# Performance work log

Hardware: AMD Instinct MI355X
Metric: run time of the kernel (lower is better)

The kernel has to match this reference:

```python
import jax, jax.numpy as jnp
import numpy as np

DIM = 256          # channel dim
WIN = 16           # window_size
PW = WIN // 2      # permuted_window_size
N = PW * PW        # tokens per window = 64
H = 8              # num_heads
KV_DIM = DIM // 2  # compressed q/k/v dim = 128
HD = KV_DIM // H   # per-head compressed dim = 16
SCALE = (DIM // H) ** (-0.5)  # NOTE: scale uses UNcompressed head dim, as in source
B = 4096           # total windows (batch * num_windows)
NW = 64            # nw_mask; B % NW == 0


def _relative_position_index():
    coords = np.stack(np.meshgrid(np.arange(PW), np.arange(PW), indexing='ij'))  # [2,PW,PW]
    cf = coords.reshape(2, -1)                          # [2, N]
    rel = cf[:, :, None] - cf[:, None, :]               # [2, N, N]
    rel = rel.transpose(1, 2, 0).copy()                 # [N, N, 2]
    rel[:, :, 0] += PW - 1
    rel[:, :, 1] += PW - 1
    rel[:, :, 0] *= 2 * PW - 1
    return jnp.asarray(rel.sum(-1), dtype=jnp.int32)    # [N, N]


def setup_inputs() -> dict:
    key = jax.random.key(0)
    ks = jax.random.split(key, 9)
    std = 0.02
    return {
        'x': jax.random.normal(ks[0], (B, N, DIM), dtype=jnp.float32),
        'mask': jax.random.normal(ks[1], (NW, N, N), dtype=jnp.float32),
        'q_w': jax.random.normal(ks[2], (KV_DIM, DIM), dtype=jnp.float32) * std,
        'q_b': jnp.zeros((KV_DIM,), dtype=jnp.float32),
        'kv_w': jax.random.normal(ks[3], (2 * KV_DIM, DIM), dtype=jnp.float32) * std,
        'kv_b': jnp.zeros((2 * KV_DIM,), dtype=jnp.float32),
        'proj_w': jax.random.normal(ks[4], (DIM, KV_DIM), dtype=jnp.float32) * std,
        'proj_b': jnp.zeros((DIM,), dtype=jnp.float32),
        'bias_table': jax.random.normal(ks[5], ((2 * PW - 1) ** 2, H), dtype=jnp.float32) * std,
        'rel_index': _relative_position_index(),
    }


def reference(x, mask, q_w, q_b, kv_w, kv_b, proj_w, proj_b, bias_table, rel_index):
    b, n, c = x.shape
    # compressed Q and KV projections
    q = (x @ q_w.T + q_b).reshape(b, n, H, HD).transpose(0, 2, 1, 3)        # [B,H,N,HD]
    kv = (x @ kv_w.T + kv_b).reshape(b, n, 2, H, HD).transpose(2, 0, 3, 1, 4)
    k, v = kv[0], kv[1]                                                     # [B,H,N,HD]
    attn = jnp.einsum('bhnd,bhmd->bhnm', q, k) * SCALE                      # [B,H,N,N]
    # relative position bias gather
    bias = bias_table[rel_index.reshape(-1)].reshape(n, n, H).transpose(2, 0, 1)  # [H,N,N]
    attn = attn + bias[None]
    # window mask add: broadcast mask over (B//NW) window-batches and heads
    attn = attn.reshape(b // NW, NW, H, n, n) + mask[None, :, None]
    attn = attn.reshape(b, H, n, n)
    attn = jax.nn.softmax(attn, axis=-1)
    out = jnp.einsum('bhnm,bhmd->bhnd', attn, v)                            # [B,H,N,HD]
    out = out.transpose(0, 2, 1, 3).reshape(b, n, KV_DIM)
    return out @ proj_w.T + proj_b                                          # [B,N,DIM]
```

## Files before the change

kernel.cpp:

```cpp
#include <hip/hip_runtime.h>
#include <hip/hip_bf16.h>


typedef unsigned short u16;
typedef short bf16x8 __attribute__((ext_vector_type(8)));
typedef short bf16x4 __attribute__((ext_vector_type(4)));
typedef float f32x4  __attribute__((ext_vector_type(4)));

__device__ __forceinline__ f32x4 mfma_bf16(bf16x8 a, bf16x8 b, f32x4 c) {
  return __builtin_amdgcn_mfma_f32_16x16x32_bf16(a, b, c, 0, 0, 0);
}
__device__ __forceinline__ f32x4 mfma16(bf16x4 a, bf16x4 b, f32x4 c) {
#if __has_builtin(__builtin_amdgcn_mfma_f32_16x16x16bf16_1k)
  return __builtin_amdgcn_mfma_f32_16x16x16bf16_1k(a, b, c, 0, 0, 0);
#else
  f32x4 d;
  asm("v_mfma_f32_16x16x16_bf16 %0, %1, %2, %3" : "=v"(d) : "v"(a), "v"(b), "v"(c));
  return d;
#endif
}

#define SCALE_F 0.1767766952966369f
#define LOG2E_F 1.4426950408889634f
#define C2F (SCALE_F * LOG2E_F)

__device__ __forceinline__ u16 f2b(float f) {
  return __builtin_bit_cast(u16, __float2bfloat16(f));
}
__device__ __forceinline__ float b2f(u16 h) {
  return __builtin_bit_cast(float, (unsigned)h << 16);
}
__device__ __forceinline__ float fexp2(float x) {
#if __has_builtin(__builtin_amdgcn_exp2f)
  return __builtin_amdgcn_exp2f(x);
#else
  return __expf(x * 0.6931471805599453f);
#endif
}

#define WS_WQKV   0
#define WS_WPROJ  98304
#define WS_BIASPK 131072
#define WS_MASKPK 163840
#define WS_QKVB   425984
#define WS_TOTAL  426368

__global__ void psa_prep(const float* __restrict__ qw, const float* __restrict__ qb,
                         const float* __restrict__ kvw, const float* __restrict__ kvb,
                         const float* __restrict__ projw, const float* __restrict__ bt,
                         const int* __restrict__ ri, const float* __restrict__ mask,
                         u16* __restrict__ ws) {
  int i = blockIdx.x * 256 + threadIdx.x;
  if (i < 98304) {
    int r = i >> 8, c = i & 255;
    ws[WS_WQKV + i] = f2b(r < 128 ? qw[r * 256 + c] : kvw[(r - 128) * 256 + c]);
  } else if (i < 131072) {
    int j = i - 98304;
    ws[WS_WPROJ + j] = f2b(projw[j]);
  } else if (i < 163840) {
    int j = i - 131072;
    int t = j & 15, lane = (j >> 4) & 63, w = (j >> 10) & 3, h = j >> 12;
    int row = w * 16 + (lane & 15);
    int col = (t >> 2) * 16 + ((lane >> 4) & 3) * 4 + (t & 3);
    ws[WS_BIASPK + j] = f2b(LOG2E_F * bt[ri[row * 64 + col] * 8 + h]);
  } else if (i < 425984) {
    int j = i - 163840;
    int t = j & 15, lane = (j >> 4) & 63, w = (j >> 10) & 3, nw = j >> 12;
    int row = w * 16 + (lane & 15);
    int col = (t >> 2) * 16 + ((lane >> 4) & 3) * 4 + (t & 3);
    ws[WS_MASKPK + j] = f2b(LOG2E_F * mask[(nw * 64 + row) * 64 + col]);
  } else if (i < WS_TOTAL) {
    int j = i - 425984;
    ws[WS_QKVB + j] = f2b(j < 128 ? qb[j] : kvb[j - 128]);
  }
}

__global__ __launch_bounds__(256, 3) void psa_main(
    const float* __restrict__ x, const float* __restrict__ proj_b,
    const u16* __restrict__ ws, float* __restrict__ out) {
  __shared__ __align__(16) u16 qks[64 * 264];
  __shared__ __align__(16) u16 vsm[8 * 16 * 72];

  const int win = blockIdx.x;
  const int tid = threadIdx.x;
  const int wave = tid >> 6;
  const int lane = tid & 63;
  const int quad = lane >> 4;
  const int n16  = lane & 15;
  const int nw   = win & 63;

  const f32x4 zero4 = {0.f, 0.f, 0.f, 0.f};
  const float* xw = x + (size_t)win * 16384;

  #pragma unroll
  for (int it = 0; it < 16; ++it) {
    int idx = it * 256 + tid;
    int row = idx >> 6, c4 = (idx & 63) * 4;
    float4 v = *(const float4*)(xw + row * 256 + c4);
    bf16x4 pk;
    pk[0] = (short)f2b(v.x); pk[1] = (short)f2b(v.y);
    pk[2] = (short)f2b(v.z); pk[3] = (short)f2b(v.w);
    *(bf16x4*)&qks[row * 264 + c4] = pk;
  }
  __syncthreads();

  f32x4 acc[6][4];
  #pragma unroll
  for (int i = 0; i < 6; ++i)
    #pragma unroll
    for (int nt = 0; nt < 4; ++nt) acc[i][nt] = zero4;

  #pragma unroll 2
  for (int kk = 0; kk < 8; ++kk) {
    bf16x8 xf[4];
    #pragma unroll
    for (int nt = 0; nt < 4; ++nt)
      xf[nt] = *(const bf16x8*)&qks[(nt * 16 + n16) * 264 + kk * 32 + quad * 8];
    #pragma unroll
    for (int i = 0; i < 6; ++i) {
      int mt = wave + i * 4;
      bf16x8 wf = *(const bf16x8*)&ws[WS_WQKV + (mt * 16 + n16) * 256 + kk * 32 + quad * 8];
      #pragma unroll
      for (int nt = 0; nt < 4; ++nt) acc[i][nt] = mfma_bf16(wf, xf[nt], acc[i][nt]);
    }
  }
  __syncthreads();

  #pragma unroll
  for (int i = 0; i < 6; ++i) {
    int mt = wave + i * 4;
    bf16x4 bq = *(const bf16x4*)&ws[WS_QKVB + mt * 16 + quad * 4];
    float ba[4];
    #pragma unroll
    for (int r = 0; r < 4; ++r) ba[r] = b2f((u16)bq[r]);
    if (i < 4) {
      #pragma unroll
      for (int nt = 0; nt < 4; ++nt) {
        bf16x4 pk;
        #pragma unroll
        for (int r = 0; r < 4; ++r) pk[r] = (short)f2b(acc[i][nt][r] + ba[r]);
        *(bf16x4*)&qks[(nt * 16 + n16) * 264 + mt * 16 + quad * 4] = pk;
      }
    } else {
      #pragma unroll
      for (int nt = 0; nt < 4; ++nt)
        #pragma unroll
        for (int r = 0; r < 4; ++r)
          vsm[(mt - 16) * 1152 + (quad * 4 + r) * 72 + nt * 16 + n16] =
              f2b(acc[i][nt][r] + ba[r]);
    }
  }
  __syncthreads();

  const u16* bpk = ws + WS_BIASPK + (wave * 64 + lane) * 16;
  const u16* mpk = ws + WS_MASKPK + ((nw * 4 + wave) * 64 + lane) * 16;
  bf16x8 mm0 = *(const bf16x8*)mpk;
  bf16x8 mm1 = *(const bf16x8*)(mpk + 8);

  #pragma unroll 2
  for (int h = 0; h < 8; ++h) {
    bf16x4 qf = *(const bf16x4*)&qks[(wave * 16 + n16) * 264 + h * 16 + quad * 4];
    f32x4 s[4];
    #pragma unroll
    for (int nt = 0; nt < 4; ++nt) {
      bf16x4 kf = *(const bf16x4*)&qks[(nt * 16 + n16) * 264 + 128 + h * 16 + quad * 4];
      s[nt] = mfma16(kf, qf, zero4);
    }
    bf16x8 bm0 = *(const bf16x8*)(bpk + h * 4096);
    bf16x8 bm1 = *(const bf16x8*)(bpk + h * 4096 + 8);

    float e[4][4];
    float psum[4];
    #pragma unroll
    for (int nt = 0; nt < 4; ++nt) {
      #pragma unroll
      for (int r = 0; r < 4; ++r) {
        int j = nt * 4 + r;
        float bv = b2f((u16)(j < 8 ? bm0[j] : bm1[j - 8]));
        float mv = b2f((u16)(j < 8 ? mm0[j] : mm1[j - 8]));
        e[nt][r] = fexp2(s[nt][r] * C2F + (bv + mv));
      }
      psum[nt] = (e[nt][0] + e[nt][1]) + (e[nt][2] + e[nt][3]);
    }
    float sum = (psum[0] + psum[1]) + (psum[2] + psum[3]);
    sum += __shfl_xor(sum, 16);
    sum += __shfl_xor(sum, 32);
    float rinv = __builtin_amdgcn_rcpf(sum);

    bf16x4 pf[4];
    #pragma unroll
    for (int nt = 0; nt < 4; ++nt) {
      bf16x4 t;
      #pragma unroll
      for (int r = 0; r < 4; ++r) t[r] = (short)f2b(e[nt][r]);
      pf[nt] = t;
    }
    f32x4 o = zero4;
    #pragma unroll
    for (int kt = 0; kt < 4; ++kt) {
      bf16x4 vf = *(const bf16x4*)&vsm[h * 1152 + n16 * 72 + kt * 16 + quad * 4];
      o = mfma16(vf, pf[kt], o);
    }
    bf16x4 ov;
    #pragma unroll
    for (int r = 0; r < 4; ++r) ov[r] = (short)f2b(o[r] * rinv);
    *(bf16x4*)&qks[(wave * 16 + n16) * 264 + h * 16 + quad * 4] = ov;
  }
  __syncthreads();

  f32x4 po[4][4];
  #pragma unroll
  for (int i = 0; i < 4; ++i)
    #pragma unroll
    for (int nt = 0; nt < 4; ++nt) po[i][nt] = zero4;
  #pragma unroll
  for (int ks = 0; ks < 4; ++ks) {
    bf16x8 of[4];
    #pragma unroll
    for (int nt = 0; nt < 4; ++nt)
      of[nt] = *(const bf16x8*)&qks[(nt * 16 + n16) * 264 + ks * 32 + quad * 8];
    #pragma unroll
    for (int i = 0; i < 4; ++i) {
      bf16x8 wf = *(const bf16x8*)&ws[WS_WPROJ + ((wave * 4 + i) * 16 + n16) * 128 + ks * 32 + quad * 8];
      #pragma unroll
      for (int nt = 0; nt < 4; ++nt) po[i][nt] = mfma_bf16(wf, of[nt], po[i][nt]);
    }
  }
  float* ow = out + (size_t)win * 16384;
  #pragma unroll
  for (int i = 0; i < 4; ++i) {
    int cbase = (wave * 4 + i) * 16 + quad * 4;
    float4 pbv = *(const float4*)(proj_b + cbase);
    #pragma unroll
    for (int nt = 0; nt < 4; ++nt) {
      int token = nt * 16 + n16;
      float4 st;
      st.x = po[i][nt][0] + pbv.x;
      st.y = po[i][nt][1] + pbv.y;
      st.z = po[i][nt][2] + pbv.z;
      st.w = po[i][nt][3] + pbv.w;
      *(float4*)(ow + token * 256 + cbase) = st;
    }
  }
}

extern "C" void kernel_launch(void* const* d_in, const int* in_sizes, int n_in,
                              void* d_out, int out_size, void* d_ws, size_t ws_size,
                              hipStream_t stream) {
  (void)in_sizes; (void)n_in; (void)out_size; (void)ws_size;
  const float* x    = (const float*)d_in[0];
  const float* mask = (const float*)d_in[1];
  const float* qw   = (const float*)d_in[2];
  const float* qb   = (const float*)d_in[3];
  const float* kvw  = (const float*)d_in[4];
  const float* kvb  = (const float*)d_in[5];
  const float* pw   = (const float*)d_in[6];
  const float* pb   = (const float*)d_in[7];
  const float* bt   = (const float*)d_in[8];
  const int*   ri   = (const int*)d_in[9];
  u16* ws = (u16*)d_ws;

  psa_prep<<<(WS_TOTAL + 255) / 256, 256, 0, stream>>>(qw, qb, kvw, kvb, pw, bt, ri, mask, ws);
  psa_main<<<4096, 256, 0, stream>>>(x, pb, ws, (float*)d_out);
}
```

Before: 580.1 us.

## Process four windows per block with register prefetch of next window input

Each block now loops over four consecutive windows. While the current window runs attention and projection, the next window's fp32 input is loaded into registers and converted to bf16 at the start of the next iteration. The aim is to hide global load latency for x and amortise block launch. The cost is a 4x smaller grid, 64 extra live VGPRs per thread with possible spills, and an added barrier per window.

```diff
diff --git a/kernel.cpp b/kernel.cpp
--- a/kernel.cpp
+++ b/kernel.cpp
@@ -75,171 +75,197 @@
   }
 }
 
+#define NWIN 4
+
 __global__ __launch_bounds__(256, 3) void psa_main(
     const float* __restrict__ x, const float* __restrict__ proj_b,
     const u16* __restrict__ ws, float* __restrict__ out) {
   __shared__ __align__(16) u16 qks[64 * 264];
   __shared__ __align__(16) u16 vsm[8 * 16 * 72];
 
-  const int win = blockIdx.x;
   const int tid = threadIdx.x;
   const int wave = tid >> 6;
   const int lane = tid & 63;
   const int quad = lane >> 4;
   const int n16  = lane & 15;
-  const int nw   = win & 63;
+  const int win0 = blockIdx.x * NWIN;
 
   const f32x4 zero4 = {0.f, 0.f, 0.f, 0.f};
-  const float* xw = x + (size_t)win * 16384;
-
-  #pragma unroll
-  for (int it = 0; it < 16; ++it) {
-    int idx = it * 256 + tid;
-    int row = idx >> 6, c4 = (idx & 63) * 4;
-    float4 v = *(const float4*)(xw + row * 256 + c4);
-    bf16x4 pk;
-    pk[0] = (short)f2b(v.x); pk[1] = (short)f2b(v.y);
-    pk[2] = (short)f2b(v.z); pk[3] = (short)f2b(v.w);
-    *(bf16x4*)&qks[row * 264 + c4] = pk;
+  const u16* bpk = ws + WS_BIASPK + (wave * 64 + lane) * 16;
+
+  float4 xp[16];
+  {
+    const float* xw = x + (size_t)win0 * 16384;
+    #pragma unroll
+    for (int it = 0; it < 16; ++it) {
+      int idx = it * 256 + tid;
+      xp[it] = *(const float4*)(xw + (idx >> 6) * 256 + (idx & 63) * 4);
+    }
   }
-  __syncthreads();
-
-  f32x4 acc[6][4];
-  #pragma unroll
-  for (int i = 0; i < 6; ++i)
-    #pragma unroll
-    for (int nt = 0; nt < 4; ++nt) acc[i][nt] = zero4;
-
-  #pragma unroll 2
-  for (int kk = 0; kk < 8; ++kk) {
-    bf16x8 xf[4];
-    #pragma unroll
-    for (int nt = 0; nt < 4; ++nt)
-      xf[nt] = *(const bf16x8*)&qks[(nt * 16 + n16) * 264 + kk * 32 + quad * 8];
+
+  #pragma unroll 1
+  for (int w = 0; w < NWIN; ++w) {
+    const int win = win0 + w;
+    const int nw  = win & 63;
+
+    #pragma unroll
+    for (int it = 0; it < 16; ++it) {
+      int idx = it * 256 + tid;
+      int row = idx >> 6, c4 = (idx & 63) * 4;
+      bf16x4 pk;
+      pk[0] = (short)f2b(xp[it].x); pk[1] = (short)f2b(xp[it].y);
+      pk[2] = (short)f2b(xp[it].z); pk[3] = (short)f2b(xp[it].w);
+      *(bf16x4*)&qks[row * 264 + c4] = pk;
+    }
+    __syncthreads();
+
+    f32x4 acc[6][4];
+    #pragma unroll
+    for (int i = 0; i < 6; ++i)
+      #pragma unroll
+      for (int nt = 0; nt < 4; ++nt) acc[i][nt] = zero4;
+
+    #pragma unroll 2
+    for (int kk = 0; kk < 8; ++kk) {
+      bf16x8 xf[4];
+      #pragma unroll
+      for (int nt = 0; nt < 4; ++nt)
+        xf[nt] = *(const bf16x8*)&qks[(nt * 16 + n16) * 264 + kk * 32 + quad * 8];
+      #pragma unroll
+      for (int i = 0; i < 6; ++i) {
+        int mt = wave + i * 4;
+        bf16x8 wf = *(const bf16x8*)&ws[WS_WQKV + (mt * 16 + n16) * 256 + kk * 32 + quad * 8];
+        #pragma unroll
+        for (int nt = 0; nt < 4; ++nt) acc[i][nt] = mfma_bf16(wf, xf[nt], acc[i][nt]);
+      }
+    }
+    __syncthreads();
+
     #pragma unroll
     for (int i = 0; i < 6; ++i) {
       int mt = wave + i * 4;
-      bf16x8 wf = *(const bf16x8*)&ws[WS_WQKV + (mt * 16 + n16) * 256 + kk * 32 + quad * 8];
-      #pragma unroll
-      for (int nt = 0; nt < 4; ++nt) acc[i][nt] = mfma_bf16(wf, xf[nt], acc[i][nt]);
-    }
-  }
-  __syncthreads();
-
-  #pragma unroll
-  for (int i = 0; i < 6; ++i) {
-    int mt = wave + i * 4;
-    bf16x4 bq = *(const bf16x4*)&ws[WS_QKVB + mt * 16 + quad * 4];
-    float ba[4];
-    #pragma unroll
-    for (int r = 0; r < 4; ++r) ba[r] = b2f((u16)bq[r]);
-    if (i < 4) {
-      #pragma unroll
-      for (int nt = 0; nt < 4; ++nt) {
-        bf16x4 pk;
-        #pragma unroll
-        for (int r = 0; r < 4; ++r) pk[r] = (short)f2b(acc[i][nt][r] + ba[r]);
-        *(bf16x4*)&qks[(nt * 16 + n16) * 264 + mt * 16 + quad * 4] = pk;
-      }
-    } else {
+      bf16x4 bq = *(const bf16x4*)&ws[WS_QKVB + mt * 16 + quad * 4];
+      float ba[4];
+      #pragma unroll
+      for (int r = 0; r < 4; ++r) ba[r] = b2f((u16)bq[r]);
+      if (i < 4) {
+        #pragma unroll
+        for (int nt = 0; nt < 4; ++nt) {
+          bf16x4 pk;
+          #pragma unroll
+          for (int r = 0; r < 4; ++r) pk[r] = (short)f2b(acc[i][nt][r] + ba[r]);
+          *(bf16x4*)&qks[(nt * 16 + n16) * 264 + mt * 16 + quad * 4] = pk;
+        }
+      } else {
+        #pragma unroll
+        for (int nt = 0; nt < 4; ++nt)
+          #pragma unroll
+          for (int r = 0; r < 4; ++r)
+            vsm[(mt - 16) * 1152 + (quad * 4 + r) * 72 + nt * 16 + n16] =
+                f2b(acc[i][nt][r] + ba[r]);
+      }
+    }
+    __syncthreads();
+
+    if (w < NWIN - 1) {
+      const float* xn = x + (size_t)(win + 1) * 16384;
+      #pragma unroll
+      for (int it = 0; it < 16; ++it) {
+        int idx = it * 256 + tid;
+        xp[it] = *(const float4*)(xn + (idx >> 6) * 256 + (idx & 63) * 4);
+      }
+    }
+
+    const u16* mpk = ws + WS_MASKPK + ((nw * 4 + wave) * 64 + lane) * 16;
+    bf16x8 mm0 = *(const bf16x8*)mpk;
+    bf16x8 mm1 = *(const bf16x8*)(mpk + 8);
+
+    #pragma unroll 2
+    for (int h = 0; h < 8; ++h) {
+      bf16x4 qf = *(const bf16x4*)&qks[(wave * 16 + n16) * 264 + h * 16 + quad * 4];
+      f32x4 s[4];
+      #pragma unroll
+      for (int nt = 0; nt < 4; ++nt) {
+        bf16x4 kf = *(const bf16x4*)&qks[(nt * 16 + n16) * 264 + 128 + h * 16 + quad * 4];
+        s[nt] = mfma16(kf, qf, zero4);
+      }
+      bf16x8 bm0 = *(const bf16x8*)(bpk + h * 4096);
+      bf16x8 bm1 = *(const bf16x8*)(bpk + h * 4096 + 8);
+
+      float e[4][4];
+      float psum[4];
+      #pragma unroll
+      for (int nt = 0; nt < 4; ++nt) {
+        #pragma unroll
+        for (int r = 0; r < 4; ++r) {
+          int j = nt * 4 + r;
+          float bv = b2f((u16)(j < 8 ? bm0[j] : bm1[j - 8]));
+          float mv = b2f((u16)(j < 8 ? mm0[j] : mm1[j - 8]));
+          e[nt][r] = fexp2(s[nt][r] * C2F + (bv + mv));
+        }
+        psum[nt] = (e[nt][0] + e[nt][1]) + (e[nt][2] + e[nt][3]);
+      }
+      float sum = (psum[0] + psum[1]) + (psum[2] + psum[3]);
+      sum += __shfl_xor(sum, 16);
+      sum += __shfl_xor(sum, 32);
+      float rinv = __builtin_amdgcn_rcpf(sum);
+
+      bf16x4 pf[4];
+      #pragma unroll
+      for (int nt = 0; nt < 4; ++nt) {
+        bf16x4 t;
+        #pragma unroll
+        for (int r = 0; r < 4; ++r) t[r] = (short)f2b(e[nt][r]);
+        pf[nt] = t;
+      }
+      f32x4 o = zero4;
+      #pragma unroll
+      for (int kt = 0; kt < 4; ++kt) {
+        bf16x4 vf = *(const bf16x4*)&vsm[h * 1152 + n16 * 72 + kt * 16 + quad * 4];
+        o = mfma16(vf, pf[kt], o);
+      }
+      bf16x4 ov;
+      #pragma unroll
+      for (int r = 0; r < 4; ++r) ov[r] = (short)f2b(o[r] * rinv);
+      *(bf16x4*)&qks[(wave * 16 + n16) * 264 + h * 16 + quad * 4] = ov;
+    }
+    __syncthreads();
+
+    f32x4 po[4][4];
+    #pragma unroll
+    for (int i = 0; i < 4; ++i)
+      #pragma unroll
+      for (int nt = 0; nt < 4; ++nt) po[i][nt] = zero4;
+    #pragma unroll
+    for (int ks = 0; ks < 4; ++ks) {
+      bf16x8 of[4];
       #pragma unroll
       for (int nt = 0; nt < 4; ++nt)
-        #pragma unroll
-        for (int r = 0; r < 4; ++r)
-          vsm[(mt - 16) * 1152 + (quad * 4 + r) * 72 + nt * 16 + n16] =
-              f2b(acc[i][nt][r] + ba[r]);
-    }
-  }
-  __syncthreads();
-
-  const u16* bpk = ws + WS_BIASPK + (wave * 64 + lane) * 16;
-  const u16* mpk = ws + WS_MASKPK + ((nw * 4 + wave) * 64 + lane) * 16;
-  bf16x8 mm0 = *(const bf16x8*)mpk;
-  bf16x8 mm1 = *(const bf16x8*)(mpk + 8);
-
-  #pragma unroll 2
-  for (int h = 0; h < 8; ++h) {
-    bf16x4 qf = *(const bf16x4*)&qks[(wave * 16 + n16) * 264 + h * 16 + quad * 4];
-    f32x4 s[4];
-    #pragma unroll
-    for (int nt = 0; nt < 4; ++nt) {
-      bf16x4 kf = *(const bf16x4*)&qks[(nt * 16 + n16) * 264 + 128 + h * 16 + quad * 4];
-      s[nt] = mfma16(kf, qf, zero4);
-    }
-    bf16x8 bm0 = *(const bf16x8*)(bpk + h * 4096);
-    bf16x8 bm1 = *(const bf16x8*)(bpk + h * 4096 + 8);
-
-    float e[4][4];
-    float psum[4];
-    #pragma unroll
-    for (int nt = 0; nt < 4; ++nt) {
-      #pragma unroll
-      for (int r = 0; r < 4; ++r) {
-        int j = nt * 4 + r;
-        float bv = b2f((u16)(j < 8 ? bm0[j] : bm1[j - 8]));
-        float mv = b2f((u16)(j < 8 ? mm0[j] : mm1[j - 8]));
-        e[nt][r] = fexp2(s[nt][r] * C2F + (bv + mv));
-      }
-      psum[nt] = (e[nt][0] + e[nt][1]) + (e[nt][2] + e[nt][3]);
-    }
-    float sum = (psum[0] + psum[1]) + (psum[2] + psum[3]);
-    sum += __shfl_xor(sum, 16);
-    sum += __shfl_xor(sum, 32);
-    float rinv = __builtin_amdgcn_rcpf(sum);
-
-    bf16x4 pf[4];
-    #pragma unroll
-    for (int nt = 0; nt < 4; ++nt) {
-      bf16x4 t;
-      #pragma unroll
-      for (int r = 0; r < 4; ++r) t[r] = (short)f2b(e[nt][r]);
-      pf[nt] = t;
-    }
-    f32x4 o = zero4;
-    #pragma unroll
-    for (int kt = 0; kt < 4; ++kt) {
-      bf16x4 vf = *(const bf16x4*)&vsm[h * 1152 + n16 * 72 + kt * 16 + quad * 4];
-      o = mfma16(vf, pf[kt], o);
-    }
-    bf16x4 ov;
-    #pragma unroll
-    for (int r = 0; r < 4; ++r) ov[r] = (short)f2b(o[r] * rinv);
-    *(bf16x4*)&qks[(wave * 16 + n16) * 264 + h * 16 + quad * 4] = ov;
-  }
-  __syncthreads();
-
-  f32x4 po[4][4];
-  #pragma unroll
-  for (int i = 0; i < 4; ++i)
-    #pragma unroll
-    for (int nt = 0; nt < 4; ++nt) po[i][nt] = zero4;
-  #pragma unroll
-  for (int ks = 0; ks < 4; ++ks) {
-    bf16x8 of[4];
-    #pragma unroll
-    for (int nt = 0; nt < 4; ++nt)
-      of[nt] = *(const bf16x8*)&qks[(nt * 16 + n16) * 264 + ks * 32 + quad * 8];
+        of[nt] = *(const bf16x8*)&qks[(nt * 16 + n16) * 264 + ks * 32 + quad * 8];
+      #pragma unroll
+      for (int i = 0; i < 4; ++i) {
+        bf16x8 wf = *(const bf16x8*)&ws[WS_WPROJ + ((wave * 4 + i) * 16 + n16) * 128 + ks * 32 + quad * 8];
+        #pragma unroll
+        for (int nt = 0; nt < 4; ++nt) po[i][nt] = mfma_bf16(wf, of[nt], po[i][nt]);
+      }
+    }
+    __syncthreads();
+
+    float* ow = out + (size_t)win * 16384;
     #pragma unroll
     for (int i = 0; i < 4; ++i) {
-      bf16x8 wf = *(const bf16x8*)&ws[WS_WPROJ + ((wave * 4 + i) * 16 + n16) * 128 + ks * 32 + quad * 8];
-      #pragma unroll
-      for (int nt = 0; nt < 4; ++nt) po[i][nt] = mfma_bf16(wf, of[nt], po[i][nt]);
-    }
-  }
-  float* ow = out + (size_t)win * 16384;
-  #pragma unroll
-  for (int i = 0; i < 4; ++i) {
-    int cbase = (wave * 4 + i) * 16 + quad * 4;
-    float4 pbv = *(const float4*)(proj_b + cbase);
-    #pragma unroll
-    for (int nt = 0; nt < 4; ++nt) {
-      int token = nt * 16 + n16;
-      float4 st;
-      st.x = po[i][nt][0] + pbv.x;
-      st.y = po[i][nt][1] + pbv.y;
-      st.z = po[i][nt][2] + pbv.z;
-      st.w = po[i][nt][3] + pbv.w;
-      *(float4*)(ow + token * 256 + cbase) = st;
+      int cbase = (wave * 4 + i) * 16 + quad * 4;
+      float4 pbv = *(const float4*)(proj_b + cbase);
+      #pragma unroll
+      for (int nt = 0; nt < 4; ++nt) {
+        int token = nt * 16 + n16;
+        float4 st;
+        st.x = po[i][nt][0] + pbv.x;
+        st.y = po[i][nt][1] + pbv.y;
+        st.z = po[i][nt][2] + pbv.z;
+        st.w = po[i][nt][3] + pbv.w;
+        *(float4*)(ow + token * 256 + cbase) = st;
+      }
     }
   }
 }
@@ -261,5 +287,5 @@
   u16* ws = (u16*)d_ws;
 
   psa_prep<<<(WS_TOTAL + 255) / 256, 256, 0, stream>>>(qw, qb, kvw, kvb, pw, bt, ri, mask, ws);
-  psa_main<<<4096, 256, 0, stream>>>(x, pb, ws, (float*)d_out);
-}
+  psa_main<<<4096 / NWIN, 256, 0, stream>>>(x, pb, ws, (float*)d_out);
+}
```

New measurement: 957.1 us. 1.65x slower.
